# Kernel optimization log

Hardware: AMD Instinct MI355X
Metric: run time of the kernel (lower is better)

The kernel has to match this reference:

```python
import jax, jax.numpy as jnp
import numpy as np

N_NODES = 50000
N_EDGES = 800000
IN_DIM = 256
HID = 32
HEADS = 4
HO = HEADS * HID  # 128
OUT_DIM = 128
EDGE_DIM = 32
L = 3
NG = 32
EPS = 1e-5


def layer_norm(x, g, b):
    mu = x.mean(-1, keepdims=True)
    var = ((x - mu) ** 2).mean(-1, keepdims=True)
    return (x - mu) / jnp.sqrt(var + EPS) * g + b


def setup_inputs() -> dict:
    key = jax.random.key(0)
    ks = jax.random.split(key, 24)

    def xav(k, shape):
        lim = np.sqrt(6.0 / (shape[-2] + shape[-1]))
        return jax.random.uniform(k, shape, minval=-lim, maxval=lim, dtype=jnp.float32)

    return {
        'x': jax.random.normal(ks[0], (N_NODES, IN_DIM), dtype=jnp.float32),
        'edge_index': jax.random.randint(ks[1], (2, N_EDGES), 0, N_NODES),
        'edge_attr': jax.random.normal(ks[2], (N_EDGES, EDGE_DIM), dtype=jnp.float32),
        'batch': jnp.sort(jax.random.randint(ks[3], (N_NODES,), 0, NG)),
        'W_in': xav(ks[4], (IN_DIM, HID)), 'b_in': jnp.zeros((HID,), jnp.float32),
        'W_ep': xav(ks[5], (EDGE_DIM, EDGE_DIM)), 'b_ep': jnp.zeros((EDGE_DIM,), jnp.float32),
        'Wq': xav(ks[6], (L, HID, HO)), 'bq': jnp.zeros((L, HO), jnp.float32),
        'Wk': xav(ks[7], (L, HID, HO)), 'bk': jnp.zeros((L, HO), jnp.float32),
        'Wv': xav(ks[8], (L, HID, HO)), 'bv': jnp.zeros((L, HO), jnp.float32),
        'We': xav(ks[9], (L, EDGE_DIM, HO)), 'be': jnp.zeros((L, HO), jnp.float32),
        'Wo': xav(ks[10], (L, HO, HID)), 'bo': jnp.zeros((L, HID), jnp.float32),
        'ln_g': jnp.ones((L, HID), jnp.float32), 'ln_b': jnp.zeros((L, HID), jnp.float32),
        'W_o1': xav(ks[11], (3 * HID, HID)), 'b_o1': jnp.zeros((HID,), jnp.float32),
        'W_o2': xav(ks[12], (HID, OUT_DIM)), 'b_o2': jnp.zeros((OUT_DIM,), jnp.float32),
    }


def gnn_forward(x, edge_index, edge_attr, batch, W_in, b_in, W_ep, b_ep,
                Wq, bq, Wk, bk, Wv, bv, We, be, Wo, bo, ln_g, ln_b,
                W_o1, b_o1, W_o2, b_o2):
    src = edge_index[0]  # source j
    dst = edge_index[1]  # target i (aggregation index)
    h = x @ W_in + b_in  # [N, HID]
    ea = edge_attr @ W_ep + b_ep  # [E, EDGE_DIM]
    scale = 1.0 / np.sqrt(HID)
    for l in range(L):
        q = (h @ Wq[l] + bq[l]).reshape(-1, HEADS, HID)
        k = (h @ Wk[l] + bk[l]).reshape(-1, HEADS, HID)
        v = (h @ Wv[l] + bv[l]).reshape(-1, HEADS, HID)
        q_i = q[dst]  # [E, H, HID]
        k_j = k[src]
        v_j = v[src]
        alpha = (q_i * k_j).sum(-1) * scale  # [E, H]
        ef = (ea @ We[l] + be[l]).reshape(-1, HEADS, HID)
        alpha = alpha + (q_i * ef).sum(-1) * scale
        # NOTE: softmax over the heads axis per edge, faithful to F.softmax(alpha, dim=-1)
        alpha = jax.nn.softmax(alpha, axis=-1)
        msg = v_j * alpha[..., None]  # [E, H, HID]
        agg = jax.ops.segment_sum(msg, dst, num_segments=N_NODES)  # [N, H, HID]
        out = agg.reshape(-1, HO) @ Wo[l] + bo[l]  # [N, HID]
        out = out + h  # residual (dims match)
        h = layer_norm(out, ln_g[l], ln_b[l])
    counts = jnp.maximum(jax.ops.segment_sum(jnp.ones((N_NODES,), h.dtype), batch, num_segments=NG), 1.0)[:, None]
    mean_pool = jax.ops.segment_sum(h, batch, num_segments=NG) / counts
    max_pool = jax.ops.segment_max(h, batch, num_segments=NG)
    gated_pool = jax.ops.segment_sum(h * jax.nn.sigmoid(h), batch, num_segments=NG) / counts
    graph_repr = jnp.concatenate([mean_pool, max_pool, gated_pool], axis=-1)  # [NG, 3*HID]
    graph_emb = jax.nn.relu(graph_repr @ W_o1 + b_o1) @ W_o2 + b_o2  # [NG, OUT_DIM]
    return graph_emb, h


def reference(x, edge_index, edge_attr, batch, W_in, b_in, W_ep, b_ep,
              Wq, bq, Wk, bk, Wv, bv, We, be, Wo, bo, ln_g, ln_b,
              W_o1, b_o1, W_o2, b_o2):
    return gnn_forward(x, edge_index, edge_attr, batch, W_in, b_in, W_ep, b_ep,
                       Wq, bq, Wk, bk, Wv, bv, We, be, Wo, bo, ln_g, ln_b,
                       W_o1, b_o1, W_o2, b_o2)
```

## Files before the change

### kernel.cpp

```cpp
#include <hip/hip_runtime.h>
#include <hip/hip_bf16.h>

#define N_NODES 50000
#define N_EDGES 800000
#define IN_DIM 256
#define HID 32
#define HEADS 4
#define HO 128
#define EDGE_DIM 32
#define NG 32
#define OUT_DIM 128
#define SCALE 0.1767766952966369f
#define SCL2  0.2550889021232886f
#define NB_SCAN ((N_NODES + 255) / 256)
#define NB_NODE ((N_NODES + 63) / 64)

typedef unsigned short u16;
typedef unsigned int u32;

__device__ __forceinline__ float bf_lo(u32 w){ union{u32 i; float f;} c; c.i=w<<16; return c.f; }
__device__ __forceinline__ float bf_hi(u32 w){ union{u32 i; float f;} c; c.i=w&0xffff0000u; return c.f; }
__device__ __forceinline__ float bf2f(u16 u){ union{u32 i; float f;} c; c.i=((u32)u)<<16; return c.f; }
__device__ __forceinline__ u16 f2bf(float f){ u32 b = __float_as_uint(f); u32 r = (b + 0x7fffu + ((b>>16)&1u)) >> 16; return (u16)r; }
__device__ __forceinline__ void bf8_store(float* d, uint4 w){
  d[0]=bf_lo(w.x); d[1]=bf_hi(w.x); d[2]=bf_lo(w.y); d[3]=bf_hi(w.y);
  d[4]=bf_lo(w.z); d[5]=bf_hi(w.z); d[6]=bf_lo(w.w); d[7]=bf_hi(w.w);
}

__global__ void k_detect(const u32* __restrict__ xw, int* __restrict__ flag){
  int lane = threadIdx.x;
  u32 w = xw[lane];
  int e_hi = (w >> 23) & 0xFF;
  int e_lo = (w >> 7) & 0xFF;
  bool pair = (e_hi >= 110 && e_hi <= 140) && (e_lo >= 110 && e_lo <= 140);
  unsigned long long m = __ballot(pair);
  if (lane == 0) flag[0] = (__popcll(m) >= 32) ? 0 : 1;
}

#define OFF_WIN   0
#define OFF_BIN   8192
#define OFF_WEP   8224
#define OFF_BEP   9248
#define OFF_WQ    9280
#define OFF_BQ    21568
#define OFF_WK    21952
#define OFF_BK    34240
#define OFF_WV    34624
#define OFF_BV    46912
#define OFF_WE    47296
#define OFF_BE    59584
#define OFF_WO    59968
#define OFF_BO    72256
#define OFF_LNG   72352
#define OFF_LNB   72448
#define OFF_WO1   72544
#define OFF_BO1   75616
#define OFF_WO2   75648
#define OFF_BO2   79744
#define TOTAL_W   79872

struct Ptrs { const void* p[20]; };

__global__ __launch_bounds__(256) void k_cvt_all(Ptrs P, const int* __restrict__ flag,
                                                 float* __restrict__ blob){
  const int offs[21] = {OFF_WIN,OFF_BIN,OFF_WEP,OFF_BEP,OFF_WQ,OFF_BQ,OFF_WK,OFF_BK,
                        OFF_WV,OFF_BV,OFF_WE,OFF_BE,OFF_WO,OFF_BO,OFF_LNG,OFF_LNB,
                        OFF_WO1,OFF_BO1,OFF_WO2,OFF_BO2,TOTAL_W};
  int isf32 = flag[0];
  int i = blockIdx.x*256 + threadIdx.x;
  if (i >= TOTAL_W) return;
  int t = 0;
  while (i >= offs[t+1]) ++t;
  int j = i - offs[t];
  float v = isf32 ? ((const float*)P.p[t])[j] : bf2f(((const u16*)P.p[t])[j]);
  blob[i] = v;
}

__global__ __launch_bounds__(256) void k_fold(const float* __restrict__ blob,
                                              float* __restrict__ M2T, float* __restrict__ bvecb){
  int l = blockIdx.x, t = threadIdx.x;
  const float* We  = blob + OFF_WE + l*HID*HO;
  const float* Wep = blob + OFF_WEP;
  const float* be  = blob + OFF_BE + l*HO;
  const float* bep = blob + OFF_BEP;
  for (int e = t; e < 4096; e += 256){
    int d = e >> 7, o = e & 127;
    int j = o & 31, hh = o >> 5;
    float s = 0.f;
    #pragma unroll
    for (int c=0; c<32; ++c) s += Wep[j*32 + c] * We[c*HO + hh*32 + d];
    M2T[l*4096 + e] = s;
  }
  if (t < HO){
    float s = be[t];
    #pragma unroll
    for (int c=0; c<32; ++c) s += bep[c] * We[c*HO + t];
    bvecb[l*HO + t] = s;
  }
}

__global__ void k_deg(const int* __restrict__ ei, int* __restrict__ deg){
  int e = blockIdx.x*256 + threadIdx.x;
  atomicAdd(&deg[ei[N_EDGES + e]], 1);
}

__global__ __launch_bounds__(256) void k_scan_a(const int* __restrict__ deg, int* __restrict__ off,
                                                int* __restrict__ bsum){
  int tid = threadIdx.x;
  int i = blockIdx.x*256 + tid;
  int d = (i < N_NODES) ? deg[i] : 0;
  int lane = tid & 63, w = tid >> 6;
  int incl = d;
  #pragma unroll
  for (int sh=1; sh<64; sh<<=1){
    int t = __shfl_up(incl, sh, 64);
    if (lane >= sh) incl += t;
  }
  __shared__ int wsum[4];
  if (lane == 63) wsum[w] = incl;
  __syncthreads();
  int wpre = 0;
  #pragma unroll
  for (int ww=0; ww<4; ++ww) wpre += (ww < w) ? wsum[ww] : 0;
  if (i < N_NODES) off[i] = wpre + incl - d;
  if (tid == 255) bsum[blockIdx.x] = wpre + incl;
}

__global__ void k_scan_b(const int* __restrict__ bsum, int* __restrict__ bpre, int* __restrict__ off){
  int lane = threadIdx.x;
  int carry = 0;
  for (int base=0; base<NB_SCAN; base+=64){
    int i = base + lane;
    int d = (i<NB_SCAN)? bsum[i] : 0;
    int incl = d;
    #pragma unroll
    for (int sh=1; sh<64; sh<<=1){
      int t = __shfl_up(incl, sh, 64);
      if (lane >= sh) incl += t;
    }
    if (i<NB_SCAN) bpre[i] = carry + incl - d;
    carry += __shfl(incl, 63, 64);
  }
  if (lane==0) off[N_NODES] = carry;
}

__global__ __launch_bounds__(256) void k_scan_c(int* __restrict__ off, const int* __restrict__ bpre){
  int i = blockIdx.x*256 + threadIdx.x;
  if (i < N_NODES) off[i] += bpre[blockIdx.x];
}

__global__ void k_fill(const int* __restrict__ ei, const int* __restrict__ off,
                       int* __restrict__ cursor, int* __restrict__ srcs, int* __restrict__ einv){
  int e = blockIdx.x*256 + threadIdx.x;
  int dst = ei[N_EDGES + e];
  int pos = atomicAdd(&cursor[dst], 1);
  int sl = off[dst] + pos;
  srcs[sl] = ei[e];
  einv[sl] = e;
}

__global__ __launch_bounds__(256) void k_eperm(const int* __restrict__ einv, const void* __restrict__ eattr,
                                               const int* __restrict__ flag, u32* __restrict__ ebf){
  int tid = blockIdx.x*256 + threadIdx.x;
  int s = tid >> 4, j = tid & 15;
  int e = einv[s];
  u32 w;
  if (flag[0]){
    float2 v2 = reinterpret_cast<const float2*>(eattr)[(size_t)e*16 + j];
    w = (u32)f2bf(v2.x) | ((u32)f2bf(v2.y) << 16);
  } else {
    w = reinterpret_cast<const u32*>(eattr)[(size_t)e*16 + j];
  }
  ebf[(size_t)s*16 + j] = w;
}

__global__ __launch_bounds__(256) void k_ghist(const int* __restrict__ batch, int* __restrict__ gcount){
  __shared__ int hist[NG];
  int tid = threadIdx.x;
  if (tid < NG) hist[tid] = 0;
  __syncthreads();
  int i = blockIdx.x*256 + tid;
  if (i < N_NODES) atomicAdd(&hist[batch[i]], 1);
  __syncthreads();
  if (tid < NG){
    int c = hist[tid];
    if (c) atomicAdd(&gcount[tid], c);
  }
}

__global__ void k_gscan(const int* __restrict__ gcount, int* __restrict__ gstart){
  int lane = threadIdx.x;
  int c = (lane < NG) ? gcount[lane] : 0;
  int incl = c;
  #pragma unroll
  for (int sh=1; sh<32; sh<<=1){
    int t = __shfl_up(incl, sh, 64);
    if (lane >= sh) incl += t;
  }
  if (lane < NG) gstart[lane] = incl - c;
}

__global__ __launch_bounds__(256) void k_embed(const void* __restrict__ xraw, const int* __restrict__ flag,
                                               const float* __restrict__ Wb, const float* __restrict__ bb,
                                               float* __restrict__ h){
  __shared__ float xs[8*IN_DIM];
  __shared__ float wsm[IN_DIM*HID];
  int tid = threadIdx.x;
  const float4* wp = reinterpret_cast<const float4*>(Wb);
  #pragma unroll
  for (int it=0; it<8; ++it) ((float4*)wsm)[it*256 + tid] = wp[it*256 + tid];
  if (flag[0]){
    const float4* xp = reinterpret_cast<const float4*>((const float*)xraw + (size_t)blockIdx.x*8*IN_DIM);
    ((float4*)xs)[tid]       = xp[tid];
    ((float4*)xs)[256 + tid] = xp[256 + tid];
  } else {
    const uint4* xp = reinterpret_cast<const uint4*>((const u16*)xraw + (size_t)blockIdx.x*8*IN_DIM);
    bf8_store(&xs[tid*8], xp[tid]);
  }
  __syncthreads();
  int nl = tid >> 5, j = tid & 31;
  float acc = bb[j];
  const float* xr = &xs[nl*IN_DIM];
  #pragma unroll 8
  for (int c=0; c<IN_DIM; ++c) acc += xr[c]*wsm[c*HID + j];
  h[(size_t)(blockIdx.x*8 + nl)*HID + j] = acc;
}

__global__ __launch_bounds__(384) void k_qkvuw2(const float* __restrict__ h,
    const float* __restrict__ blob, const float* __restrict__ M2T,
    const float* __restrict__ bvecb, int l,
    float* __restrict__ q, u32* __restrict__ kpk, u32* __restrict__ vpk,
    float* __restrict__ uw, float* __restrict__ bias4){
  __shared__ float qs[64*HO];
  int tid = threadIdx.x;
  int w = tid >> 6, lane = tid & 63;
  int hh = lane >> 4, t = lane & 15;
  int c0 = hh*32 + 2*t;
  int c1 = c0 + 1;
  {
    int m = w >> 1, half = w & 1;
    const float* Wm = blob + (m==0 ? OFF_WQ : m==1 ? OFF_WK : OFF_WV) + l*HID*HO;
    const float* bm = blob + (m==0 ? OFF_BQ : m==1 ? OFF_BK : OFF_BV) + l*HO;
    float wA[HID], wB[HID];
    #pragma unroll
    for (int c=0; c<HID; ++c){ wA[c] = Wm[c*HO + c0]; wB[c] = Wm[c*HO + c1]; }
    float bA = bm[c0], bB = bm[c1];
    u32* pk = (m==1) ? kpk : vpk;
    int n0 = blockIdx.x*64 + half*32;
    int nend = n0 + 32; if (nend > N_NODES) nend = N_NODES;
    #pragma unroll 2
    for (int n=n0; n<nend; ++n){
      const float4* hp = reinterpret_cast<const float4*>(h + (size_t)n*HID);
      float accA = bA, accB = bB;
      #pragma unroll
      for (int c4=0; c4<8; ++c4){
        float4 hv = hp[c4];
        accA += hv.x*wA[c4*4+0] + hv.y*wA[c4*4+1] + hv.z*wA[c4*4+2] + hv.w*wA[c4*4+3];
        accB += hv.x*wB[c4*4+0] + hv.y*wB[c4*4+1] + hv.z*wB[c4*4+2] + hv.w*wB[c4*4+3];
      }
      if (m==0){
        *reinterpret_cast<float2*>(q + (size_t)n*HO + c0) = make_float2(accA, accB);
        int loc = half*32 + (n - n0);
        qs[loc*HO + c0] = accA;
        qs[loc*HO + c1] = accB;
      } else {
        pk[(size_t)n*64 + lane] = (u32)f2bf(accA) | ((u32)f2bf(accB) << 16);
      }
    }
  }
  __syncthreads();
  {
    const float* M2l = M2T + l*4096;
    float m2A[HID], m2B[HID];
    #pragma unroll
    for (int d=0; d<HID; ++d){
      m2A[d] = M2l[d*HO + c0];
      m2B[d] = M2l[d*HO + c1];
    }
    float bv0 = bvecb[l*HO + c0], bv1 = bvecb[l*HO + c1];
    int nbase = blockIdx.x*64;
    for (int i = w; i < 64; i += 6){
      int n = nbase + i;
      if (n >= N_NODES) break;
      const float* qrow = &qs[i*HO];
      const float4* qh = reinterpret_cast<const float4*>(qrow + hh*32);
      float a0 = 0.f, a1 = 0.f;
      #pragma unroll
      for (int c4=0; c4<8; ++c4){
        float4 v = qh[c4];
        a0 += v.x*m2A[c4*4+0] + v.y*m2A[c4*4+1] + v.z*m2A[c4*4+2] + v.w*m2A[c4*4+3];
        a1 += v.x*m2B[c4*4+0] + v.y*m2B[c4*4+1] + v.z*m2B[c4*4+2] + v.w*m2B[c4*4+3];
      }
      float pb = qrow[c0]*bv0 + qrow[c1]*bv1;
      pb += __shfl_xor(pb, 1);
      pb += __shfl_xor(pb, 2);
      pb += __shfl_xor(pb, 4);
      pb += __shfl_xor(pb, 8);
      *reinterpret_cast<float2*>(uw + (size_t)n*HO + c0) = make_float2(a0, a1);
      if (t == 0) bias4[(size_t)n*HEADS + hh] = pb;
    }
  }
}

__global__ __launch_bounds__(256) void k_attn_agg(const int* __restrict__ off,
    const int* __restrict__ srcs,
    const float* __restrict__ q, const u32* __restrict__ kpk, const u32* __restrict__ vpk,
    const float* __restrict__ uw, const float* __restrict__ bias4,
    const u32* __restrict__ ebf,
    const float* __restrict__ Wo, const float* __restrict__ bo,
    const float* __restrict__ lng, const float* __restrict__ lnb,
    int l, int last, float* __restrict__ h, float* __restrict__ hout){
  __shared__ float aggs[4][HO];
  int tid = threadIdx.x;
  int wv = tid >> 6;
  int L  = tid & 63;
  int n = blockIdx.x*4 + wv;
  int hh = L >> 4, t = L & 15;
  int c0 = hh*32 + 2*t;
  int s0 = off[n], s1 = off[n+1];
  float2 qp = *reinterpret_cast<const float2*>(q  + (size_t)n*HO + c0);
  float2 wp = *reinterpret_cast<const float2*>(uw + (size_t)n*HO + c0);
  float4 B = reinterpret_cast<const float4*>(bias4)[n];
  float bg = (hh==0)? B.x : (hh==1)? B.y : (hh==2)? B.z : B.w;
  float acc0=0.f, acc1=0.f;
  auto proc = [&](u32 kw, u32 vw, u32 ew){
    float pa = qp.x*bf_lo(kw) + qp.y*bf_hi(kw) + wp.x*bf_lo(ew) + wp.y*bf_hi(ew);
    pa += __shfl_xor(pa, 1);
    pa += __shfl_xor(pa, 2);
    pa += __shfl_xor(pa, 4);
    pa += __shfl_xor(pa, 8);
    float e = exp2f((pa + bg)*SCL2);
    float ssum = e + __shfl_xor(e, 16);
    ssum += __shfl_xor(ssum, 32);
    float wgt = e * __builtin_amdgcn_rcpf(ssum);
    acc0 += bf_lo(vw)*wgt;
    acc1 += bf_hi(vw)*wgt;
  };
  int s = s0;
  for (; s + 4 <= s1; s += 4){
    int sn0 = srcs[s], sn1 = srcs[s+1], sn2 = srcs[s+2], sn3 = srcs[s+3];
    u32 kw0 = kpk[(size_t)sn0*64 + L], vw0 = vpk[(size_t)sn0*64 + L];
    u32 kw1 = kpk[(size_t)sn1*64 + L], vw1 = vpk[(size_t)sn1*64 + L];
    u32 kw2 = kpk[(size_t)sn2*64 + L], vw2 = vpk[(size_t)sn2*64 + L];
    u32 kw3 = kpk[(size_t)sn3*64 + L], vw3 = vpk[(size_t)sn3*64 + L];
    u32 ew0 = ebf[(size_t)s*16 + t],       ew1 = ebf[(size_t)(s+1)*16 + t];
    u32 ew2 = ebf[(size_t)(s+2)*16 + t],   ew3 = ebf[(size_t)(s+3)*16 + t];
    proc(kw0, vw0, ew0);
    proc(kw1, vw1, ew1);
    proc(kw2, vw2, ew2);
    proc(kw3, vw3, ew3);
  }
  for (; s < s1; ++s){
    int sn = srcs[s];
    proc(kpk[(size_t)sn*64 + L], vpk[(size_t)sn*64 + L], ebf[(size_t)s*16 + t]);
  }
  *reinterpret_cast<float2*>(&aggs[wv][c0]) = make_float2(acc0, acc1);
  __syncthreads();
  if (tid < 128){
    int nl2 = tid >> 5, j = tid & 31;
    int nn = blockIdx.x*4 + nl2;
    const float* Wol = Wo + l*HO*HID;
    float o = bo[l*HID + j];
    #pragma unroll
    for (int i=0; i<HO; ++i) o += aggs[nl2][i] * Wol[i*HID + j];
    o += h[(size_t)nn*HID + j];
    float sum = o;
    #pragma unroll
    for (int m=16; m>=1; m>>=1) sum += __shfl_xor(sum, m);
    float mu = sum * (1.f/32.f);
    float dv = o - mu;
    float vs = dv*dv;
    #pragma unroll
    for (int m=16; m>=1; m>>=1) vs += __shfl_xor(vs, m);
    float xn = dv * rsqrtf(vs*(1.f/32.f) + 1e-5f);
    float res = xn * lng[l*HID + j] + lnb[l*HID + j];
    h[(size_t)nn*HID + j] = res;
    if (last) hout[(size_t)nn*HID + j] = res;
  }
}

__global__ __launch_bounds__(256) void k_pool(const float* __restrict__ h, const int* __restrict__ gstart,
                                              const int* __restrict__ gcount, float* __restrict__ pools){
  int g = blockIdx.x;
  int start = gstart[g], cnt = gcount[g];
  int tid = threadIdx.x;
  int sub = tid >> 5, j = tid & 31;
  float sum = 0.f, mx = -1e30f, gs = 0.f;
  for (int i = start + sub; i < start + cnt; i += 8){
    float val = h[(size_t)i*HID + j];
    sum += val;
    mx = fmaxf(mx, val);
    gs += val * (1.0f/(1.0f + __expf(-val)));
  }
  __shared__ float ls[8][HID], lm[8][HID], lg[8][HID];
  ls[sub][j]=sum; lm[sub][j]=mx; lg[sub][j]=gs;
  __syncthreads();
  if (tid < HID){
    float S=0.f, M=-1e30f, G=0.f;
    #pragma unroll
    for (int s2=0; s2<8; ++s2){ S+=ls[s2][tid]; M=fmaxf(M,lm[s2][tid]); G+=lg[s2][tid]; }
    float c = (float)((cnt>0)?cnt:1);
    pools[g*96 + tid]      = S/c;
    pools[g*96 + 32 + tid] = M;
    pools[g*96 + 64 + tid] = G/c;
  }
}

__global__ __launch_bounds__(128) void k_head(const float* __restrict__ pools,
    const float* __restrict__ Wo1, const float* __restrict__ bo1,
    const float* __restrict__ Wo2, const float* __restrict__ bo2,
    float* __restrict__ out){
  int g = blockIdx.x, tid = threadIdx.x;
  __shared__ float rep[96], hid[HID];
  if (tid < 96) rep[tid] = pools[g*96 + tid];
  __syncthreads();
  if (tid < HID){
    float s = bo1[tid];
    #pragma unroll
    for (int c=0; c<96; ++c) s += rep[c]*Wo1[c*HID + tid];
    hid[tid] = fmaxf(s, 0.0f);
  }
  __syncthreads();
  float s = bo2[tid];
  #pragma unroll
  for (int j2=0; j2<HID; ++j2) s += hid[j2]*Wo2[j2*OUT_DIM + tid];
  out[g*OUT_DIM + tid] = s;
}

extern "C" void kernel_launch(void* const* d_in, const int* in_sizes, int n_in,
                              void* d_out, int out_size, void* d_ws, size_t ws_size,
                              hipStream_t stream){
  const void* x     = d_in[0];
  const int*  ei    = (const int*)d_in[1];
  const void* eattr = d_in[2];
  const int*  batch = (const int*)d_in[3];
  float* out = (float*)d_out;

  char* p = (char*)d_ws;
  auto take = [&](size_t bytes)->char*{ char* r = p; p += (bytes + 255) & ~(size_t)255; return r; };
  float* h     = (float*)take((size_t)N_NODES*HID*4);
  float* q     = (float*)take((size_t)N_NODES*HO*4);
  u32*   kpk   = (u32*)  take((size_t)N_NODES*64*4);
  u32*   vpk   = (u32*)  take((size_t)N_NODES*64*4);
  float* uw    = (float*)take((size_t)N_NODES*HO*4);
  float* bias4 = (float*)take((size_t)N_NODES*HEADS*4);
  char* zbase  = take((size_t)N_NODES*4 + 256 + (size_t)N_NODES*4 + 256 + NG*4);
  int* deg     = (int*)zbase;
  int* cursor  = (int*)(zbase + (((size_t)N_NODES*4 + 255) & ~(size_t)255));
  int* gcount  = (int*)((char*)cursor + (((size_t)N_NODES*4 + 255) & ~(size_t)255));
  size_t zspan = ((char*)gcount + NG*4) - zbase;
  int* off     = (int*)take((size_t)(N_NODES+1)*4);
  int* srcs    = (int*)take((size_t)N_EDGES*4);
  int* einv    = (int*)take((size_t)N_EDGES*4);
  int* gstart  = (int*)take(NG*4);
  float* pools = (float*)take(NG*96*4);
  int*   flag  = (int*)take(256);
  int*   bsum  = (int*)take(NB_SCAN*4);
  int*   bpre  = (int*)take(NB_SCAN*4);
  float* blob  = (float*)take((size_t)TOTAL_W*4);
  float* M2T   = (float*)take((size_t)3*4096*4);
  float* bvecb = (float*)take((size_t)3*HO*4);
  u32*   ebf   = (u32*)  take((size_t)N_EDGES*16*4);
  (void)ws_size; (void)in_sizes; (void)n_in; (void)out_size;

  Ptrs P;
  for (int i=0; i<20; ++i) P.p[i] = d_in[4+i];

  k_detect<<<1, 64, 0, stream>>>((const u32*)x, flag);
  k_cvt_all<<<(TOTAL_W+255)/256, 256, 0, stream>>>(P, flag, blob);
  k_fold<<<3, 256, 0, stream>>>(blob, M2T, bvecb);

  hipMemsetAsync(zbase, 0, zspan, stream);
  k_deg <<<N_EDGES/256, 256, 0, stream>>>(ei, deg);
  k_scan_a<<<NB_SCAN, 256, 0, stream>>>(deg, off, bsum);
  k_scan_b<<<1, 64, 0, stream>>>(bsum, bpre, off);
  k_scan_c<<<NB_SCAN, 256, 0, stream>>>(off, bpre);
  k_fill<<<N_EDGES/256, 256, 0, stream>>>(ei, off, cursor, srcs, einv);
  k_eperm<<<(N_EDGES*16)/256, 256, 0, stream>>>(einv, eattr, flag, ebf);
  k_ghist<<<NB_SCAN, 256, 0, stream>>>(batch, gcount);
  k_gscan<<<1, 64, 0, stream>>>(gcount, gstart);
  k_embed<<<N_NODES/8, 256, 0, stream>>>(x, flag, blob+OFF_WIN, blob+OFF_BIN, h);
  for (int l=0; l<3; ++l){
    k_qkvuw2<<<NB_NODE, 384, 0, stream>>>(h, blob, M2T, bvecb, l, q, kpk, vpk, uw, bias4);
    k_attn_agg<<<N_NODES/4, 256, 0, stream>>>(off, srcs, q, kpk, vpk, uw, bias4, ebf,
                                              blob+OFF_WO, blob+OFF_BO, blob+OFF_LNG, blob+OFF_LNB,
                                              l, (l==2)?1:0, h, out + NG*OUT_DIM);
  }
  k_pool<<<NG, 256, 0, stream>>>(h, gstart, gcount, pools);
  k_head<<<NG, 128, 0, stream>>>(pools, blob+OFF_WO1, blob+OFF_BO1, blob+OFF_WO2, blob+OFF_BO2, out);
}
```

Measured before the change: 789.5 us.

## Fuse prep kernels, interleave K/V rows, and unroll edge gather by eight

Merges dtype detection, weight conversion and the edge-weight fold into one prep kernel, with the dtype check recomputed per wave instead of stored in a flag. The graph histogram moves into the scan kernel, and the group prefix is computed inside the pool kernel, which removes several tiny launches. K and V are stored interleaved per node so each neighbor's k and v words share a 512-byte row. The attention gather loop is unrolled to eight edges to keep more loads in flight, at the cost of more registers.

```diff
diff --git a/kernel.cpp b/kernel.cpp
--- a/kernel.cpp
+++ b/kernel.cpp
@@ -14,6 +14,7 @@
 #define SCL2  0.2550889021232886f
 #define NB_SCAN ((N_NODES + 255) / 256)
 #define NB_NODE ((N_NODES + 63) / 64)
+#define NB_CVT  312
 
 typedef unsigned short u16;
 typedef unsigned int u32;
@@ -27,14 +28,12 @@
   d[4]=bf_lo(w.z); d[5]=bf_hi(w.z); d[6]=bf_lo(w.w); d[7]=bf_hi(w.w);
 }
 
-__global__ void k_detect(const u32* __restrict__ xw, int* __restrict__ flag){
-  int lane = threadIdx.x;
-  u32 w = xw[lane];
+__device__ __forceinline__ int wave_isf32(const u32* __restrict__ xw){
+  u32 w = xw[threadIdx.x & 63];
   int e_hi = (w >> 23) & 0xFF;
   int e_lo = (w >> 7) & 0xFF;
   bool pair = (e_hi >= 110 && e_hi <= 140) && (e_lo >= 110 && e_lo <= 140);
-  unsigned long long m = __ballot(pair);
-  if (lane == 0) flag[0] = (__popcll(m) >= 32) ? 0 : 1;
+  return (__popcll(__ballot(pair)) >= 32) ? 0 : 1;
 }
 
 #define OFF_WIN   0
@@ -61,41 +60,45 @@
 
 struct Ptrs { const void* p[20]; };
 
-__global__ __launch_bounds__(256) void k_cvt_all(Ptrs P, const int* __restrict__ flag,
-                                                 float* __restrict__ blob){
-  const int offs[21] = {OFF_WIN,OFF_BIN,OFF_WEP,OFF_BEP,OFF_WQ,OFF_BQ,OFF_WK,OFF_BK,
-                        OFF_WV,OFF_BV,OFF_WE,OFF_BE,OFF_WO,OFF_BO,OFF_LNG,OFF_LNB,
-                        OFF_WO1,OFF_BO1,OFF_WO2,OFF_BO2,TOTAL_W};
-  int isf32 = flag[0];
-  int i = blockIdx.x*256 + threadIdx.x;
-  if (i >= TOTAL_W) return;
-  int t = 0;
-  while (i >= offs[t+1]) ++t;
-  int j = i - offs[t];
-  float v = isf32 ? ((const float*)P.p[t])[j] : bf2f(((const u16*)P.p[t])[j]);
-  blob[i] = v;
-}
-
-__global__ __launch_bounds__(256) void k_fold(const float* __restrict__ blob,
+__global__ __launch_bounds__(256) void k_prep(Ptrs P, const u32* __restrict__ xw,
+                                              float* __restrict__ blob,
                                               float* __restrict__ M2T, float* __restrict__ bvecb){
-  int l = blockIdx.x, t = threadIdx.x;
-  const float* We  = blob + OFF_WE + l*HID*HO;
-  const float* Wep = blob + OFF_WEP;
-  const float* be  = blob + OFF_BE + l*HO;
-  const float* bep = blob + OFF_BEP;
-  for (int e = t; e < 4096; e += 256){
-    int d = e >> 7, o = e & 127;
-    int j = o & 31, hh = o >> 5;
-    float s = 0.f;
-    #pragma unroll
-    for (int c=0; c<32; ++c) s += Wep[j*32 + c] * We[c*HO + hh*32 + d];
-    M2T[l*4096 + e] = s;
-  }
-  if (t < HO){
-    float s = be[t];
-    #pragma unroll
-    for (int c=0; c<32; ++c) s += bep[c] * We[c*HO + t];
-    bvecb[l*HO + t] = s;
+  int isf32 = wave_isf32(xw);
+  int b = blockIdx.x;
+  if (b < NB_CVT){
+    const int offs[21] = {OFF_WIN,OFF_BIN,OFF_WEP,OFF_BEP,OFF_WQ,OFF_BQ,OFF_WK,OFF_BK,
+                          OFF_WV,OFF_BV,OFF_WE,OFF_BE,OFF_WO,OFF_BO,OFF_LNG,OFF_LNB,
+                          OFF_WO1,OFF_BO1,OFF_WO2,OFF_BO2,TOTAL_W};
+    int i = b*256 + threadIdx.x;
+    if (i >= TOTAL_W) return;
+    int t = 0;
+    while (i >= offs[t+1]) ++t;
+    int j = i - offs[t];
+    blob[i] = isf32 ? ((const float*)P.p[t])[j] : bf2f(((const u16*)P.p[t])[j]);
+  } else {
+    int l = b - NB_CVT;
+    const void* We  = P.p[10];
+    const void* Wep = P.p[2];
+    const void* be  = P.p[11];
+    const void* bep = P.p[3];
+    auto ld = [&](const void* q2, int idx)->float{
+      return isf32 ? ((const float*)q2)[idx] : bf2f(((const u16*)q2)[idx]);
+    };
+    int t = threadIdx.x;
+    for (int e = t; e < 4096; e += 256){
+      int d = e >> 7, o = e & 127;
+      int j = o & 31, hh = o >> 5;
+      float s = 0.f;
+      #pragma unroll
+      for (int c=0; c<32; ++c) s += ld(Wep, j*32 + c) * ld(We, l*HID*HO + c*HO + hh*32 + d);
+      M2T[l*4096 + e] = s;
+    }
+    if (t < HO){
+      float s = ld(be, l*HO + t);
+      #pragma unroll
+      for (int c=0; c<32; ++c) s += ld(bep, c) * ld(We, l*HID*HO + c*HO + t);
+      bvecb[l*HO + t] = s;
+    }
   }
 }
 
@@ -105,8 +108,12 @@
 }
 
 __global__ __launch_bounds__(256) void k_scan_a(const int* __restrict__ deg, int* __restrict__ off,
-                                                int* __restrict__ bsum){
+                                                int* __restrict__ bsum,
+                                                const int* __restrict__ batch, int* __restrict__ gcount){
+  __shared__ int wsum[4];
+  __shared__ int hist[NG];
   int tid = threadIdx.x;
+  if (tid < NG) hist[tid] = 0;
   int i = blockIdx.x*256 + tid;
   int d = (i < N_NODES) ? deg[i] : 0;
   int lane = tid & 63, w = tid >> 6;
@@ -116,7 +123,6 @@
     int t = __shfl_up(incl, sh, 64);
     if (lane >= sh) incl += t;
   }
-  __shared__ int wsum[4];
   if (lane == 63) wsum[w] = incl;
   __syncthreads();
   int wpre = 0;
@@ -124,6 +130,12 @@
   for (int ww=0; ww<4; ++ww) wpre += (ww < w) ? wsum[ww] : 0;
   if (i < N_NODES) off[i] = wpre + incl - d;
   if (tid == 255) bsum[blockIdx.x] = wpre + incl;
+  if (i < N_NODES) atomicAdd(&hist[batch[i]], 1);
+  __syncthreads();
+  if (tid < NG){
+    int c = hist[tid];
+    if (c) atomicAdd(&gcount[tid], c);
+  }
 }
 
 __global__ void k_scan_b(const int* __restrict__ bsum, int* __restrict__ bpre, int* __restrict__ off){
@@ -160,12 +172,13 @@
 }
 
 __global__ __launch_bounds__(256) void k_eperm(const int* __restrict__ einv, const void* __restrict__ eattr,
-                                               const int* __restrict__ flag, u32* __restrict__ ebf){
+                                               const u32* __restrict__ xw, u32* __restrict__ ebf){
+  int isf32 = wave_isf32(xw);
   int tid = blockIdx.x*256 + threadIdx.x;
   int s = tid >> 4, j = tid & 15;
   int e = einv[s];
   u32 w;
-  if (flag[0]){
+  if (isf32){
     float2 v2 = reinterpret_cast<const float2*>(eattr)[(size_t)e*16 + j];
     w = (u32)f2bf(v2.x) | ((u32)f2bf(v2.y) << 16);
   } else {
@@ -174,42 +187,17 @@
   ebf[(size_t)s*16 + j] = w;
 }
 
-__global__ __launch_bounds__(256) void k_ghist(const int* __restrict__ batch, int* __restrict__ gcount){
-  __shared__ int hist[NG];
-  int tid = threadIdx.x;
-  if (tid < NG) hist[tid] = 0;
-  __syncthreads();
-  int i = blockIdx.x*256 + tid;
-  if (i < N_NODES) atomicAdd(&hist[batch[i]], 1);
-  __syncthreads();
-  if (tid < NG){
-    int c = hist[tid];
-    if (c) atomicAdd(&gcount[tid], c);
-  }
-}
-
-__global__ void k_gscan(const int* __restrict__ gcount, int* __restrict__ gstart){
-  int lane = threadIdx.x;
-  int c = (lane < NG) ? gcount[lane] : 0;
-  int incl = c;
-  #pragma unroll
-  for (int sh=1; sh<32; sh<<=1){
-    int t = __shfl_up(incl, sh, 64);
-    if (lane >= sh) incl += t;
-  }
-  if (lane < NG) gstart[lane] = incl - c;
-}
-
-__global__ __launch_bounds__(256) void k_embed(const void* __restrict__ xraw, const int* __restrict__ flag,
+__global__ __launch_bounds__(256) void k_embed(const void* __restrict__ xraw,
                                                const float* __restrict__ Wb, const float* __restrict__ bb,
                                                float* __restrict__ h){
   __shared__ float xs[8*IN_DIM];
   __shared__ float wsm[IN_DIM*HID];
+  int isf32 = wave_isf32((const u32*)xraw);
   int tid = threadIdx.x;
   const float4* wp = reinterpret_cast<const float4*>(Wb);
   #pragma unroll
   for (int it=0; it<8; ++it) ((float4*)wsm)[it*256 + tid] = wp[it*256 + tid];
-  if (flag[0]){
+  if (isf32){
     const float4* xp = reinterpret_cast<const float4*>((const float*)xraw + (size_t)blockIdx.x*8*IN_DIM);
     ((float4*)xs)[tid]       = xp[tid];
     ((float4*)xs)[256 + tid] = xp[256 + tid];
@@ -229,7 +217,7 @@
 __global__ __launch_bounds__(384) void k_qkvuw2(const float* __restrict__ h,
     const float* __restrict__ blob, const float* __restrict__ M2T,
     const float* __restrict__ bvecb, int l,
-    float* __restrict__ q, u32* __restrict__ kpk, u32* __restrict__ vpk,
+    float* __restrict__ q, u32* __restrict__ kv,
     float* __restrict__ uw, float* __restrict__ bias4){
   __shared__ float qs[64*HO];
   int tid = threadIdx.x;
@@ -245,7 +233,7 @@
     #pragma unroll
     for (int c=0; c<HID; ++c){ wA[c] = Wm[c*HO + c0]; wB[c] = Wm[c*HO + c1]; }
     float bA = bm[c0], bB = bm[c1];
-    u32* pk = (m==1) ? kpk : vpk;
+    int voff = (m==1) ? 0 : 64;
     int n0 = blockIdx.x*64 + half*32;
     int nend = n0 + 32; if (nend > N_NODES) nend = N_NODES;
     #pragma unroll 2
@@ -264,7 +252,7 @@
         qs[loc*HO + c0] = accA;
         qs[loc*HO + c1] = accB;
       } else {
-        pk[(size_t)n*64 + lane] = (u32)f2bf(accA) | ((u32)f2bf(accB) << 16);
+        kv[(size_t)n*128 + voff + lane] = (u32)f2bf(accA) | ((u32)f2bf(accB) << 16);
       }
     }
   }
@@ -304,7 +292,7 @@
 
 __global__ __launch_bounds__(256) void k_attn_agg(const int* __restrict__ off,
     const int* __restrict__ srcs,
-    const float* __restrict__ q, const u32* __restrict__ kpk, const u32* __restrict__ vpk,
+    const float* __restrict__ q, const u32* __restrict__ kv,
     const float* __restrict__ uw, const float* __restrict__ bias4,
     const u32* __restrict__ ebf,
     const float* __restrict__ Wo, const float* __restrict__ bo,
@@ -337,22 +325,41 @@
     acc1 += bf_hi(vw)*wgt;
   };
   int s = s0;
-  for (; s + 4 <= s1; s += 4){
-    int sn0 = srcs[s], sn1 = srcs[s+1], sn2 = srcs[s+2], sn3 = srcs[s+3];
-    u32 kw0 = kpk[(size_t)sn0*64 + L], vw0 = vpk[(size_t)sn0*64 + L];
-    u32 kw1 = kpk[(size_t)sn1*64 + L], vw1 = vpk[(size_t)sn1*64 + L];
-    u32 kw2 = kpk[(size_t)sn2*64 + L], vw2 = vpk[(size_t)sn2*64 + L];
-    u32 kw3 = kpk[(size_t)sn3*64 + L], vw3 = vpk[(size_t)sn3*64 + L];
-    u32 ew0 = ebf[(size_t)s*16 + t],       ew1 = ebf[(size_t)(s+1)*16 + t];
-    u32 ew2 = ebf[(size_t)(s+2)*16 + t],   ew3 = ebf[(size_t)(s+3)*16 + t];
-    proc(kw0, vw0, ew0);
-    proc(kw1, vw1, ew1);
-    proc(kw2, vw2, ew2);
-    proc(kw3, vw3, ew3);
+  for (; s + 8 <= s1; s += 8){
+    int sn[8];
+    u32 kw[8], vw[8], ew[8];
+    #pragma unroll
+    for (int u=0; u<8; ++u) sn[u] = srcs[s+u];
+    #pragma unroll
+    for (int u=0; u<8; ++u){
+      const u32* base = kv + (size_t)sn[u]*128;
+      kw[u] = base[L];
+      vw[u] = base[64 + L];
+      ew[u] = ebf[(size_t)(s+u)*16 + t];
+    }
+    #pragma unroll
+    for (int u=0; u<8; ++u) proc(kw[u], vw[u], ew[u]);
+  }
+  if (s + 4 <= s1){
+    int sn[4];
+    u32 kw[4], vw[4], ew[4];
+    #pragma unroll
+    for (int u=0; u<4; ++u) sn[u] = srcs[s+u];
+    #pragma unroll
+    for (int u=0; u<4; ++u){
+      const u32* base = kv + (size_t)sn[u]*128;
+      kw[u] = base[L];
+      vw[u] = base[64 + L];
+      ew[u] = ebf[(size_t)(s+u)*16 + t];
+    }
+    #pragma unroll
+    for (int u=0; u<4; ++u) proc(kw[u], vw[u], ew[u]);
+    s += 4;
   }
   for (; s < s1; ++s){
     int sn = srcs[s];
-    proc(kpk[(size_t)sn*64 + L], vpk[(size_t)sn*64 + L], ebf[(size_t)s*16 + t]);
+    const u32* base = kv + (size_t)sn*128;
+    proc(base[L], base[64 + L], ebf[(size_t)s*16 + t]);
   }
   *reinterpret_cast<float2*>(&aggs[wv][c0]) = make_float2(acc0, acc1);
   __syncthreads();
@@ -379,11 +386,16 @@
   }
 }
 
-__global__ __launch_bounds__(256) void k_pool(const float* __restrict__ h, const int* __restrict__ gstart,
+__global__ __launch_bounds__(256) void k_pool(const float* __restrict__ h,
                                               const int* __restrict__ gcount, float* __restrict__ pools){
+  __shared__ int gc[NG];
   int g = blockIdx.x;
-  int start = gstart[g], cnt = gcount[g];
   int tid = threadIdx.x;
+  if (tid < NG) gc[tid] = gcount[tid];
+  __syncthreads();
+  int start = 0;
+  for (int g2=0; g2<g; ++g2) start += gc[g2];
+  int cnt = gc[g];
   int sub = tid >> 5, j = tid & 31;
   float sum = 0.f, mx = -1e30f, gs = 0.f;
   for (int i = start + sub; i < start + cnt; i += 8){
@@ -440,8 +452,7 @@
   auto take = [&](size_t bytes)->char*{ char* r = p; p += (bytes + 255) & ~(size_t)255; return r; };
   float* h     = (float*)take((size_t)N_NODES*HID*4);
   float* q     = (float*)take((size_t)N_NODES*HO*4);
-  u32*   kpk   = (u32*)  take((size_t)N_NODES*64*4);
-  u32*   vpk   = (u32*)  take((size_t)N_NODES*64*4);
+  u32*   kv    = (u32*)  take((size_t)N_NODES*128*4);
   float* uw    = (float*)take((size_t)N_NODES*HO*4);
   float* bias4 = (float*)take((size_t)N_NODES*HEADS*4);
   char* zbase  = take((size_t)N_NODES*4 + 256 + (size_t)N_NODES*4 + 256 + NG*4);
@@ -452,9 +463,7 @@
   int* off     = (int*)take((size_t)(N_NODES+1)*4);
   int* srcs    = (int*)take((size_t)N_EDGES*4);
   int* einv    = (int*)take((size_t)N_EDGES*4);
-  int* gstart  = (int*)take(NG*4);
   float* pools = (float*)take(NG*96*4);
-  int*   flag  = (int*)take(256);
   int*   bsum  = (int*)take(NB_SCAN*4);
   int*   bpre  = (int*)take(NB_SCAN*4);
   float* blob  = (float*)take((size_t)TOTAL_W*4);
@@ -466,26 +475,21 @@
   Ptrs P;
   for (int i=0; i<20; ++i) P.p[i] = d_in[4+i];
 
-  k_detect<<<1, 64, 0, stream>>>((const u32*)x, flag);
-  k_cvt_all<<<(TOTAL_W+255)/256, 256, 0, stream>>>(P, flag, blob);
-  k_fold<<<3, 256, 0, stream>>>(blob, M2T, bvecb);
-
+  k_prep<<<NB_CVT + 3, 256, 0, stream>>>(P, (const u32*)x, blob, M2T, bvecb);
   hipMemsetAsync(zbase, 0, zspan, stream);
   k_deg <<<N_EDGES/256, 256, 0, stream>>>(ei, deg);
-  k_scan_a<<<NB_SCAN, 256, 0, stream>>>(deg, off, bsum);
+  k_scan_a<<<NB_SCAN, 256, 0, stream>>>(deg, off, bsum, batch, gcount);
   k_scan_b<<<1, 64, 0, stream>>>(bsum, bpre, off);
   k_scan_c<<<NB_SCAN, 256, 0, stream>>>(off, bpre);
   k_fill<<<N_EDGES/256, 256, 0, stream>>>(ei, off, cursor, srcs, einv);
-  k_eperm<<<(N_EDGES*16)/256, 256, 0, stream>>>(einv, eattr, flag, ebf);
-  k_ghist<<<NB_SCAN, 256, 0, stream>>>(batch, gcount);
-  k_gscan<<<1, 64, 0, stream>>>(gcount, gstart);
-  k_embed<<<N_NODES/8, 256, 0, stream>>>(x, flag, blob+OFF_WIN, blob+OFF_BIN, h);
+  k_eperm<<<(N_EDGES*16)/256, 256, 0, stream>>>(einv, eattr, (const u32*)x, ebf);
+  k_embed<<<N_NODES/8, 256, 0, stream>>>(x, blob+OFF_WIN, blob+OFF_BIN, h);
   for (int l=0; l<3; ++l){
-    k_qkvuw2<<<NB_NODE, 384, 0, stream>>>(h, blob, M2T, bvecb, l, q, kpk, vpk, uw, bias4);
-    k_attn_agg<<<N_NODES/4, 256, 0, stream>>>(off, srcs, q, kpk, vpk, uw, bias4, ebf,
+    k_qkvuw2<<<NB_NODE, 384, 0, stream>>>(h, blob, M2T, bvecb, l, q, kv, uw, bias4);
+    k_attn_agg<<<N_NODES/4, 256, 0, stream>>>(off, srcs, q, kv, uw, bias4, ebf,
                                               blob+OFF_WO, blob+OFF_BO, blob+OFF_LNG, blob+OFF_LNB,
                                               l, (l==2)?1:0, h, out + NG*OUT_DIM);
   }
-  k_pool<<<NG, 256, 0, stream>>>(h, gstart, gcount, pools);
+  k_pool<<<NG, 256, 0, stream>>>(h, gcount, pools);
   k_head<<<NG, 128, 0, stream>>>(pools, blob+OFF_WO1, blob+OFF_BO1, blob+OFF_WO2, blob+OFF_BO2, out);
 }
```

Result: slower. 852.4 us (+8.0%).
